# Optimization experiments

Hardware: AMD Instinct MI355X
Metric: run time of the kernel (lower is better)

Reference implementation:

```python
import jax, jax.numpy as jnp
import numpy as np

N = 2500   # total_neurons
K = 50     # connections_per_neuron
T = 60     # temporal_sequence
F = 5      # input_features
H = 128    # lstm hidden_size
B = 512    # batch
GROUPS = [800, 700, 600, 400]  # support_resistance, trend_detection, pattern_recognition, volume_analysis


def _lstm_layer(x, Wih, Whh, bih, bhh):
    # x: [B, T, D]; PyTorch gate order (i, f, g, o); eval mode (no dropout)
    bs = x.shape[0]
    h0 = jnp.zeros((bs, H), x.dtype)

    def step(carry, xt):
        h, c = carry
        g = xt @ Wih.T + h @ Whh.T + bih + bhh
        i, f, gg, o = jnp.split(g, 4, axis=-1)
        c = jax.nn.sigmoid(f) * c + jax.nn.sigmoid(i) * jnp.tanh(gg)
        h = jax.nn.sigmoid(o) * jnp.tanh(c)
        return (h, c), h

    (h, c), ys = jax.lax.scan(step, (h0, h0), jnp.swapaxes(x, 0, 1))
    return jnp.swapaxes(ys, 0, 1), h


def _forward(x, W_ih0, W_hh0, b_ih0, b_hh0, W_ih1, W_hh1, b_ih1, b_hh1,
             fp_w1, fp_b1, fp_w2, fp_b2, conn_w, sens, thr,
             int_w1, int_b1, int_w2, int_b2, int_w3, int_b3,
             tw, tb, pw, pb, kw, kb, vw, vb, cw, cb, conn_idx):
    y0, _ = _lstm_layer(x, W_ih0, W_hh0, b_ih0, b_hh0)
    _, hlast = _lstm_layer(y0, W_ih1, W_hh1, b_ih1, b_hh1)        # hidden[-1]: [B, H]
    base = jnp.tanh(jax.nn.relu(hlast @ fp_w1.T + fp_b1) @ fp_w2.T + fp_b2)  # [B, 32]
    # all_activations = base repeated over N neurons; each neuron reduces its
    # K gathered activations (weighted) and the identical 32 feature dims to a scalar.
    feat_sum = base.sum(-1)                                        # [B]
    acts = jnp.broadcast_to(feat_sum[:, None], (x.shape[0], N))    # [B, N]
    gathered = acts[:, conn_idx]                                   # [B, N, K] irregular gather
    wi = jnp.einsum('bnk,nk->bn', gathered, conn_w)                # [B, N]
    pre = wi * sens
    o0 = GROUPS[0]; o1 = o0 + GROUPS[1]; o2 = o1 + GROUPS[2]
    neuron_out = jnp.concatenate([
        jax.nn.sigmoid(pre[:, :o0] - thr[:o0]),                    # support_resistance
        jnp.tanh(pre[:, o0:o1]),                                   # trend_detection
        jax.nn.relu(pre[:, o1:o2] - thr[o1:o2]),                   # pattern_recognition
        jax.nn.sigmoid(pre[:, o2:]),                               # volume_analysis
    ], axis=1)                                                     # [B, N]
    h1 = jax.nn.relu(neuron_out @ int_w1.T + int_b1)
    h2 = jax.nn.relu(h1 @ int_w2.T + int_b2)
    integrated = jnp.tanh(h2 @ int_w3.T + int_b3)                  # [B, 32]
    trend = integrated @ tw.T + tb                                 # [B, 3]
    patt = integrated @ pw.T + pb                                  # [B, 6]
    keyl = integrated @ kw.T + kb                                  # [B, 4]
    vol = integrated @ vw.T + vb                                   # [B, 1]
    conf = integrated @ cw.T + cb                                  # [B, 1]
    means = jnp.stack([neuron_out[:, :o0].mean(1), neuron_out[:, o0:o1].mean(1),
                       neuron_out[:, o1:o2].mean(1), neuron_out[:, o2:].mean(1)], axis=-1)
    # heads(15) + raw confidence(1) + overall_confidence(1) + specialty means(4) -> [B, 21]? no: 3+6+4+1+1+1+4 = 20
    return jnp.concatenate([trend, patt, keyl, vol, conf, jax.nn.sigmoid(conf), means], axis=-1)


def setup_inputs() -> dict:
    key = jax.random.key(0)
    ks = jax.random.split(key, 40)
    rn = lambda k, s, sc=0.1: jax.random.normal(k, s, dtype=jnp.float32) * sc
    inp = {}
    inp['x'] = jax.random.normal(ks[0], (B, T, F), dtype=jnp.float32)
    inp['W_ih0'] = rn(ks[1], (4 * H, F)); inp['W_hh0'] = rn(ks[2], (4 * H, H))
    inp['b_ih0'] = rn(ks[3], (4 * H,));   inp['b_hh0'] = rn(ks[4], (4 * H,))
    inp['W_ih1'] = rn(ks[5], (4 * H, H)); inp['W_hh1'] = rn(ks[6], (4 * H, H))
    inp['b_ih1'] = rn(ks[7], (4 * H,));   inp['b_hh1'] = rn(ks[8], (4 * H,))
    inp['fp_w1'] = rn(ks[9], (64, H));    inp['fp_b1'] = rn(ks[10], (64,))
    inp['fp_w2'] = rn(ks[11], (32, 64));  inp['fp_b2'] = rn(ks[12], (32,))
    inp['conn_w'] = rn(ks[13], (N, K))
    inp['sens'] = 1.0 + rn(ks[14], (N,))
    inp['thr'] = 0.6 + rn(ks[15], (N,))
    inp['int_w1'] = rn(ks[16], (256, N), 0.02); inp['int_b1'] = rn(ks[17], (256,))
    inp['int_w2'] = rn(ks[18], (64, 256));      inp['int_b2'] = rn(ks[19], (64,))
    inp['int_w3'] = rn(ks[20], (32, 64));       inp['int_b3'] = rn(ks[21], (32,))
    inp['tw'] = rn(ks[22], (3, 32)); inp['tb'] = rn(ks[23], (3,))
    inp['pw'] = rn(ks[24], (6, 32)); inp['pb'] = rn(ks[25], (6,))
    inp['kw'] = rn(ks[26], (4, 32)); inp['kb'] = rn(ks[27], (4,))
    inp['vw'] = rn(ks[28], (1, 32)); inp['vb'] = rn(ks[29], (1,))
    inp['cw'] = rn(ks[30], (1, 32)); inp['cb'] = rn(ks[31], (1,))
    inp['conn_idx'] = jax.random.randint(ks[32], (N, K), 0, N)
    return inp


def reference(x, W_ih0, W_hh0, b_ih0, b_hh0, W_ih1, W_hh1, b_ih1, b_hh1,
              fp_w1, fp_b1, fp_w2, fp_b2, conn_w, sens, thr,
              int_w1, int_b1, int_w2, int_b2, int_w3, int_b3,
              tw, tb, pw, pb, kw, kb, vw, vb, cw, cb, conn_idx):
    return _forward(x, W_ih0, W_hh0, b_ih0, b_hh0, W_ih1, W_hh1, b_ih1, b_hh1,
                    fp_w1, fp_b1, fp_w2, fp_b2, conn_w, sens, thr,
                    int_w1, int_b1, int_w2, int_b2, int_w3, int_b3,
                    tw, tb, pw, pb, kw, kb, vw, vb, cw, cb, conn_idx)
```

## Files before the change

### kernel.cpp

```cpp
#include <hip/hip_runtime.h>
#include <math.h>

#define NB   512
#define TT   60
#define FF   5
#define HH   128
#define G4   512
#define NN   2500
#define KK   50

#define O0 800
#define O1 1500
#define O2 2100

#define OFF_B0F   0
#define OFF_B1F   40960
#define OFF_XA    106496
#define OFF_BIAS0 598016
#define OFF_BIAS1 598528
#define OFF_A     599040
#define OFF_FS    601540
#define OFF_MEANS 602052
#define OFF_H1    604100

#define PREP_T0 81920
#define PREP_T1 212992
#define PREP_T2 1196032
#define PREP_T3 1196544
#define PREP_T4 1197056
#define PREP_TOTAL 1199556

typedef _Float16 f16x8 __attribute__((ext_vector_type(8)));
typedef float f32x4 __attribute__((ext_vector_type(4)));

__device__ __forceinline__ float sigf(float x) {
    return 1.0f / (1.0f + __expf(-x));
}
__device__ __forceinline__ float tanh2(float x) {
    float e = __expf(-2.0f * x);
    return fmaf(2.0f, 1.0f / (1.0f + e), -1.0f);
}

__global__ __launch_bounds__(256) void prep_kernel(
    const float* __restrict__ x,
    const float* __restrict__ W_ih0, const float* __restrict__ W_hh0,
    const float* __restrict__ b_ih0, const float* __restrict__ b_hh0,
    const float* __restrict__ W_ih1, const float* __restrict__ W_hh1,
    const float* __restrict__ b_ih1, const float* __restrict__ b_hh1,
    const float* __restrict__ conn_w, const float* __restrict__ sens,
    float* __restrict__ ws)
{
    int i = blockIdx.x * 256 + threadIdx.x;
    if (i >= PREP_TOTAL) return;

    if (i < PREP_T0) {
        int j = i & 7, l = (i >> 3) & 63;
        int rest = i >> 9;
        int g = rest & 3;
        int kbw = rest >> 2;
        int kb = kbw % 5, w = kbw / 5;
        int k = kb * 32 + (l >> 4) * 8 + j;
        int n = g * 128 + w * 16 + (l & 15);
        float val = 0.f;
        if (k < 128)       val = W_hh0[n * HH + k];
        else if (k < 133)  val = W_ih0[n * FF + (k - 128)];
        ((_Float16*)(ws + OFF_B0F))[i] = (_Float16)val;
    } else if (i < PREP_T1) {
        int v = i - PREP_T0;
        int j = v & 7, l = (v >> 3) & 63;
        int rest = v >> 9;
        int g = rest & 3;
        int kb = (rest >> 2) & 7;
        int w = rest >> 5;
        int k = kb * 32 + (l >> 4) * 8 + j;
        int n = g * 128 + w * 16 + (l & 15);
        float val = (k < 128) ? W_ih1[n * HH + k] : W_hh1[n * HH + (k - 128)];
        ((_Float16*)(ws + OFF_B1F))[v] = (_Float16)val;
    } else if (i < PREP_T2) {
        int v = i - PREP_T1;
        int j = v & 7, l = (v >> 3) & 63;
        int rest = v >> 9;
        int t = rest % 60, bb = rest / 60;
        float val = 0.f;
        if (l < 16 && j < 5)
            val = x[(bb * 16 + (l & 15)) * (TT * FF) + t * FF + j];
        ((_Float16*)(ws + OFF_XA))[v] = (_Float16)val;
    } else if (i < PREP_T3) {
        int j = i - PREP_T2;
        ws[OFF_BIAS0 + j] = b_ih0[j] + b_hh0[j];
    } else if (i < PREP_T4) {
        int j = i - PREP_T3;
        ws[OFF_BIAS1 + j] = b_ih1[j] + b_hh1[j];
    } else {
        int n = i - PREP_T4;
        float s = 0.f;
        const float* cw = conn_w + n * KK;
        for (int k = 0; k < KK; ++k) s += cw[k];
        ws[OFF_A + n] = s * sens[n];
    }
}

__global__ __launch_bounds__(512) void lstm_mfma(
    const float* __restrict__ ws_ro,
    const float* __restrict__ fp_w1, const float* __restrict__ fp_b1,
    const float* __restrict__ fp_w2, const float* __restrict__ fp_b2,
    float* __restrict__ feat_sum)
{
    __shared__ __align__(16) _Float16 hcat[8 * 512];
    __shared__ float t1s[16][65];
    __shared__ float bss[16][33];

    const int tid = threadIdx.x;
    const int w = tid >> 6, l = tid & 63;
    const int u = w * 16 + (l & 15);
    const int row0 = (l >> 4) * 4;
    const int bb = blockIdx.x;

    ((uint4*)hcat)[tid] = make_uint4(0u, 0u, 0u, 0u);

    float bia0[4], bia1[4];
#pragma unroll
    for (int g = 0; g < 4; ++g) {
        bia0[g] = ws_ro[OFF_BIAS0 + g * 128 + u];
        bia1[g] = ws_ro[OFF_BIAS1 + g * 128 + u];
    }
    float c0[4] = {0.f, 0.f, 0.f, 0.f};
    float c1[4] = {0.f, 0.f, 0.f, 0.f};

    const f16x8* B0 = (const f16x8*)(ws_ro + OFF_B0F) + w * 20 * 64 + l;
    const f16x8* B1 = (const f16x8*)(ws_ro + OFF_B1F) + w * 32 * 64 + l;
    const f16x8* XA = (const f16x8*)(ws_ro + OFF_XA) + bb * 60 * 64 + l;
    const f16x8* HF = (const f16x8*)hcat;

    const int h0base = (u >> 5) * 512 + ((u >> 3) & 3) * 128 + (u & 7);
    const int h1base = h0base + 2048;

    __syncthreads();

    for (int t = 0; t < TT; ++t) {
        f32x4 a0 = {0.f,0.f,0.f,0.f}, a1 = {0.f,0.f,0.f,0.f};
        f32x4 a2 = {0.f,0.f,0.f,0.f}, a3 = {0.f,0.f,0.f,0.f};
        f16x8 xaf = XA[t * 64];
#pragma unroll
        for (int kb = 0; kb < 4; ++kb) {
            f16x8 af = HF[kb * 64 + l];
            a0 = __builtin_amdgcn_mfma_f32_16x16x32_f16(af, B0[(kb*4+0)*64], a0, 0,0,0);
            a1 = __builtin_amdgcn_mfma_f32_16x16x32_f16(af, B0[(kb*4+1)*64], a1, 0,0,0);
            a2 = __builtin_amdgcn_mfma_f32_16x16x32_f16(af, B0[(kb*4+2)*64], a2, 0,0,0);
            a3 = __builtin_amdgcn_mfma_f32_16x16x32_f16(af, B0[(kb*4+3)*64], a3, 0,0,0);
        }
        a0 = __builtin_amdgcn_mfma_f32_16x16x32_f16(xaf, B0[(16+0)*64], a0, 0,0,0);
        a1 = __builtin_amdgcn_mfma_f32_16x16x32_f16(xaf, B0[(16+1)*64], a1, 0,0,0);
        a2 = __builtin_amdgcn_mfma_f32_16x16x32_f16(xaf, B0[(16+2)*64], a2, 0,0,0);
        a3 = __builtin_amdgcn_mfma_f32_16x16x32_f16(xaf, B0[(16+3)*64], a3, 0,0,0);

        float h0v[4];
#pragma unroll
        for (int r = 0; r < 4; ++r) {
            float gi = sigf(a0[r] + bia0[0]);
            float gf = sigf(a1[r] + bia0[1]);
            float gg = tanh2(a2[r] + bia0[2]);
            float go = sigf(a3[r] + bia0[3]);
            c0[r] = gf * c0[r] + gi * gg;
            h0v[r] = go * tanh2(c0[r]);
        }
        __syncthreads();
#pragma unroll
        for (int r = 0; r < 4; ++r)
            hcat[h0base + (row0 + r) * 8] = (_Float16)h0v[r];
        __syncthreads();

        f32x4 b0a = {0.f,0.f,0.f,0.f}, b1a = {0.f,0.f,0.f,0.f};
        f32x4 b2a = {0.f,0.f,0.f,0.f}, b3a = {0.f,0.f,0.f,0.f};
#pragma unroll
        for (int kb = 0; kb < 8; ++kb) {
            f16x8 af = HF[kb * 64 + l];
            b0a = __builtin_amdgcn_mfma_f32_16x16x32_f16(af, B1[(kb*4+0)*64], b0a, 0,0,0);
            b1a = __builtin_amdgcn_mfma_f32_16x16x32_f16(af, B1[(kb*4+1)*64], b1a, 0,0,0);
            b2a = __builtin_amdgcn_mfma_f32_16x16x32_f16(af, B1[(kb*4+2)*64], b2a, 0,0,0);
            b3a = __builtin_amdgcn_mfma_f32_16x16x32_f16(af, B1[(kb*4+3)*64], b3a, 0,0,0);
        }
        float h1v[4];
#pragma unroll
        for (int r = 0; r < 4; ++r) {
            float gi = sigf(b0a[r] + bia1[0]);
            float gf = sigf(b1a[r] + bia1[1]);
            float gg = tanh2(b2a[r] + bia1[2]);
            float go = sigf(b3a[r] + bia1[3]);
            c1[r] = gf * c1[r] + gi * gg;
            h1v[r] = go * tanh2(c1[r]);
        }
        __syncthreads();
#pragma unroll
        for (int r = 0; r < 4; ++r)
            hcat[h1base + (row0 + r) * 8] = (_Float16)h1v[r];
        __syncthreads();
    }

    for (int idx = tid; idx < 16 * 64; idx += 512) {
        int r = idx >> 6, m = idx & 63;
        float acc = fp_b1[m];
        const float* wp = fp_w1 + m * HH;
        for (int k = 0; k < HH; ++k) {
            float hv = (float)hcat[(4 + (k >> 5)) * 512 +
                                   (r + ((k >> 3) & 3) * 16) * 8 + (k & 7)];
            acc = fmaf(wp[k], hv, acc);
        }
        t1s[r][m] = fmaxf(acc, 0.f);
    }
    __syncthreads();
    if (tid < 16 * 32) {
        int r = tid >> 5, q = tid & 31;
        float acc = fp_b2[q];
        const float* wp = fp_w2 + q * 64;
        for (int m = 0; m < 64; ++m) acc = fmaf(wp[m], t1s[r][m], acc);
        bss[r][q] = tanh2(acc);
    }
    __syncthreads();
    if (tid < 16) {
        float s = 0.f;
        for (int q = 0; q < 32; ++q) s += bss[tid][q];
        feat_sum[bb * 16 + tid] = s;
    }
}

__device__ __forceinline__ float actn(int n, float pre, float th) {
    if (n < O0)       return sigf(pre - th);
    else if (n < O1)  return tanh2(pre);
    else if (n < O2)  return fmaxf(pre - th, 0.f);
    else              return sigf(pre);
}

__global__ __launch_bounds__(256) void means_kernel(
    const float* __restrict__ feat_sum, const float* __restrict__ a,
    const float* __restrict__ thr, float* __restrict__ means)
{
    const int b = blockIdx.x;
    const float s = feat_sum[b];
    float g0 = 0.f, g1 = 0.f, g2 = 0.f, g3 = 0.f;
    for (int n = threadIdx.x; n < NN; n += 256) {
        float v = actn(n, s * a[n], thr[n]);
        if (n < O0) g0 += v; else if (n < O1) g1 += v;
        else if (n < O2) g2 += v; else g3 += v;
    }
    __shared__ float red[4][256];
    red[0][threadIdx.x] = g0; red[1][threadIdx.x] = g1;
    red[2][threadIdx.x] = g2; red[3][threadIdx.x] = g3;
    __syncthreads();
    if (threadIdx.x < 4) {
        float acc = 0.f;
        for (int i = 0; i < 256; ++i) acc += red[threadIdx.x][i];
        const float inv[4] = {1.f/800.f, 1.f/700.f, 1.f/600.f, 1.f/400.f};
        means[b * 4 + threadIdx.x] = acc * inv[threadIdx.x];
    }
}

__global__ __launch_bounds__(256) void gemm_h1(
    const float* __restrict__ feat_sum,
    const float* __restrict__ aw, const float* __restrict__ thr,
    const float* __restrict__ int_w1,
    const float* __restrict__ int_b1,
    float* __restrict__ h1)
{
    __shared__ float As[32][33];
    __shared__ float Bs[32][33];
    const int b0 = blockIdx.x * 32;
    const int m0 = blockIdx.y * 32;
    const int tid = threadIdx.x;
    const int ty = tid >> 4, tx = tid & 15;
    const int li = tid >> 3;
    const int lj = (tid & 7) * 4;

    const float s_li = feat_sum[b0 + li];

    float acc00 = 0.f, acc01 = 0.f, acc10 = 0.f, acc11 = 0.f;

    for (int k0 = 0; k0 < NN; k0 += 32) {
        float4 av = make_float4(0.f, 0.f, 0.f, 0.f);
        if (k0 + lj < NN) {
            float4 aa = *(const float4*)(aw + k0 + lj);
            float4 tt = *(const float4*)(thr + k0 + lj);
            int n = k0 + lj;
            av.x = actn(n + 0, s_li * aa.x, tt.x);
            av.y = actn(n + 1, s_li * aa.y, tt.y);
            av.z = actn(n + 2, s_li * aa.z, tt.z);
            av.w = actn(n + 3, s_li * aa.w, tt.w);
        }
        As[li][lj + 0] = av.x; As[li][lj + 1] = av.y;
        As[li][lj + 2] = av.z; As[li][lj + 3] = av.w;

        float4 wv = make_float4(0.f, 0.f, 0.f, 0.f);
        if (k0 + lj < NN)
            wv = *(const float4*)(int_w1 + (m0 + li) * NN + k0 + lj);
        Bs[lj + 0][li] = wv.x; Bs[lj + 1][li] = wv.y;
        Bs[lj + 2][li] = wv.z; Bs[lj + 3][li] = wv.w;
        __syncthreads();

#pragma unroll 8
        for (int kk = 0; kk < 32; ++kk) {
            float a0 = As[ty * 2][kk],  a1 = As[ty * 2 + 1][kk];
            float w0 = Bs[kk][tx * 2],  w1 = Bs[kk][tx * 2 + 1];
            acc00 += a0 * w0; acc01 += a0 * w1;
            acc10 += a1 * w0; acc11 += a1 * w1;
        }
        __syncthreads();
    }
    const int bi = b0 + ty * 2, mj = m0 + tx * 2;
    h1[bi * 256 + mj]           = fmaxf(acc00 + int_b1[mj], 0.f);
    h1[bi * 256 + mj + 1]       = fmaxf(acc01 + int_b1[mj + 1], 0.f);
    h1[(bi + 1) * 256 + mj]     = fmaxf(acc10 + int_b1[mj], 0.f);
    h1[(bi + 1) * 256 + mj + 1] = fmaxf(acc11 + int_b1[mj + 1], 0.f);
}

__global__ __launch_bounds__(64) void tail_kernel(
    const float* __restrict__ h1,
    const float* __restrict__ int_w2, const float* __restrict__ int_b2,
    const float* __restrict__ int_w3, const float* __restrict__ int_b3,
    const float* __restrict__ tw, const float* __restrict__ tb,
    const float* __restrict__ pw, const float* __restrict__ pb,
    const float* __restrict__ kw, const float* __restrict__ kb,
    const float* __restrict__ vw, const float* __restrict__ vb,
    const float* __restrict__ cw, const float* __restrict__ cb,
    const float* __restrict__ means,
    float* __restrict__ out)
{
    const int b = blockIdx.x;
    const int lane = threadIdx.x;
    __shared__ float h2s[64];
    __shared__ float ints[32];
    __shared__ float outs[16];

    {
        float acc = int_b2[lane];
        const float* hp = h1 + b * 256;
        const float* wp = int_w2 + lane * 256;
        for (int m = 0; m < 256; ++m) acc += wp[m] * hp[m];
        h2s[lane] = fmaxf(acc, 0.f);
    }
    __syncthreads();
    if (lane < 32) {
        float acc = int_b3[lane];
        const float* wp = int_w3 + lane * 64;
        for (int m = 0; m < 64; ++m) acc += wp[m] * h2s[m];
        ints[lane] = tanh2(acc);
    }
    __syncthreads();
    if (lane < 15) {
        const float* wsel; float bsel;
        if (lane < 3)       { wsel = tw + lane * 32;       bsel = tb[lane]; }
        else if (lane < 9)  { wsel = pw + (lane - 3) * 32; bsel = pb[lane - 3]; }
        else if (lane < 13) { wsel = kw + (lane - 9) * 32; bsel = kb[lane - 9]; }
        else if (lane == 13){ wsel = vw;                   bsel = vb[0]; }
        else                { wsel = cw;                   bsel = cb[0]; }
        float acc = bsel;
        for (int q = 0; q < 32; ++q) acc += wsel[q] * ints[q];
        outs[lane] = acc;
    }
    __syncthreads();
    if (lane < 20) {
        float v;
        if (lane < 15)       v = outs[lane];
        else if (lane == 15) v = sigf(outs[14]);
        else                 v = means[b * 4 + (lane - 16)];
        out[b * 20 + lane] = v;
    }
}

extern "C" void kernel_launch(void* const* d_in, const int* in_sizes, int n_in,
                              void* d_out, int out_size, void* d_ws, size_t ws_size,
                              hipStream_t stream)
{
    const float* x      = (const float*)d_in[0];
    const float* W_ih0  = (const float*)d_in[1];
    const float* W_hh0  = (const float*)d_in[2];
    const float* b_ih0  = (const float*)d_in[3];
    const float* b_hh0  = (const float*)d_in[4];
    const float* W_ih1  = (const float*)d_in[5];
    const float* W_hh1  = (const float*)d_in[6];
    const float* b_ih1  = (const float*)d_in[7];
    const float* b_hh1  = (const float*)d_in[8];
    const float* fp_w1  = (const float*)d_in[9];
    const float* fp_b1  = (const float*)d_in[10];
    const float* fp_w2  = (const float*)d_in[11];
    const float* fp_b2  = (const float*)d_in[12];
    const float* conn_w = (const float*)d_in[13];
    const float* sens   = (const float*)d_in[14];
    const float* thr    = (const float*)d_in[15];
    const float* int_w1 = (const float*)d_in[16];
    const float* int_b1 = (const float*)d_in[17];
    const float* int_w2 = (const float*)d_in[18];
    const float* int_b2 = (const float*)d_in[19];
    const float* int_w3 = (const float*)d_in[20];
    const float* int_b3 = (const float*)d_in[21];
    const float* tw     = (const float*)d_in[22];
    const float* tb     = (const float*)d_in[23];
    const float* pw     = (const float*)d_in[24];
    const float* pb     = (const float*)d_in[25];
    const float* kw     = (const float*)d_in[26];
    const float* kb     = (const float*)d_in[27];
    const float* vw     = (const float*)d_in[28];
    const float* vb     = (const float*)d_in[29];
    const float* cw     = (const float*)d_in[30];
    const float* cb     = (const float*)d_in[31];

    float* ws = (float*)d_ws;
    float* out = (float*)d_out;

    prep_kernel<<<(PREP_TOTAL + 255) / 256, 256, 0, stream>>>(
        x, W_ih0, W_hh0, b_ih0, b_hh0, W_ih1, W_hh1, b_ih1, b_hh1,
        conn_w, sens, ws);

    lstm_mfma<<<NB / 16, 512, 0, stream>>>(
        ws, fp_w1, fp_b1, fp_w2, fp_b2, ws + OFF_FS);

    means_kernel<<<NB, 256, 0, stream>>>(
        ws + OFF_FS, ws + OFF_A, thr, ws + OFF_MEANS);

    {
        dim3 grid(NB / 32, 256 / 32);
        gemm_h1<<<grid, 256, 0, stream>>>(
            ws + OFF_FS, ws + OFF_A, thr, int_w1, int_b1, ws + OFF_H1);
    }

    tail_kernel<<<NB, 64, 0, stream>>>(
        ws + OFF_H1, int_w2, int_b2, int_w3, int_b3,
        tw, tb, pw, pb, kw, kb, vw, vb, cw, cb,
        ws + OFF_MEANS, out);
}
```

Before: 392.4 us.

## Double-buffer LSTM hidden state, keep layer-0 weights in registers, fuse means into tail

The hidden-state LDS buffer is now double-buffered, so each LSTM timestep writes its h values directly after the gate math. That cuts the per-step barriers from four to two. Layer-0 weight fragments are kept in registers for the whole sequence, and layer-1 weight loads and the next input slice are prefetched one step ahead. The separate means kernel is removed and its reduction folded into the tail kernel, saving a launch. The risks are higher register pressure from the 20 cached fragments with the occupancy hint of two, and a smaller 64-thread block doing the 2500-neuron reduction.

```diff
diff --git a/kernel.cpp b/kernel.cpp
--- a/kernel.cpp
+++ b/kernel.cpp
@@ -20,8 +20,7 @@
 #define OFF_BIAS1 598528
 #define OFF_A     599040
 #define OFF_FS    601540
-#define OFF_MEANS 602052
-#define OFF_H1    604100
+#define OFF_H1    602052
 
 #define PREP_T0 81920
 #define PREP_T1 212992
@@ -100,13 +99,13 @@
     }
 }
 
-__global__ __launch_bounds__(512) void lstm_mfma(
+__global__ __launch_bounds__(512, 2) void lstm_mfma(
     const float* __restrict__ ws_ro,
     const float* __restrict__ fp_w1, const float* __restrict__ fp_b1,
     const float* __restrict__ fp_w2, const float* __restrict__ fp_b2,
     float* __restrict__ feat_sum)
 {
-    __shared__ __align__(16) _Float16 hcat[8 * 512];
+    __shared__ __align__(16) _Float16 hcat[2 * 4096];
     __shared__ float t1s[16][65];
     __shared__ float bss[16][33];
 
@@ -132,29 +131,41 @@
     const f16x8* XA = (const f16x8*)(ws_ro + OFF_XA) + bb * 60 * 64 + l;
     const f16x8* HF = (const f16x8*)hcat;
 
+    f16x8 wb0[20];
+#pragma unroll
+    for (int i = 0; i < 20; ++i) wb0[i] = B0[i * 64];
+
     const int h0base = (u >> 5) * 512 + ((u >> 3) & 3) * 128 + (u & 7);
     const int h1base = h0base + 2048;
 
-    __syncthreads();
-
-    for (int t = 0; t < TT; ++t) {
+    f16x8 xa = XA[0];
+
+    __syncthreads();
+
+    auto step = [&](int SRC, int DST, int t) {
+        const f16x8* hs = HF + SRC * 512;
+        const f16x8* hd = HF + DST * 512;
+        _Float16* hw = hcat + DST * 4096;
+
+        f16x8 xan = XA[(t + 1 < TT ? t + 1 : TT - 1) * 64];
+
         f32x4 a0 = {0.f,0.f,0.f,0.f}, a1 = {0.f,0.f,0.f,0.f};
         f32x4 a2 = {0.f,0.f,0.f,0.f}, a3 = {0.f,0.f,0.f,0.f};
-        f16x8 xaf = XA[t * 64];
 #pragma unroll
         for (int kb = 0; kb < 4; ++kb) {
-            f16x8 af = HF[kb * 64 + l];
-            a0 = __builtin_amdgcn_mfma_f32_16x16x32_f16(af, B0[(kb*4+0)*64], a0, 0,0,0);
-            a1 = __builtin_amdgcn_mfma_f32_16x16x32_f16(af, B0[(kb*4+1)*64], a1, 0,0,0);
-            a2 = __builtin_amdgcn_mfma_f32_16x16x32_f16(af, B0[(kb*4+2)*64], a2, 0,0,0);
-            a3 = __builtin_amdgcn_mfma_f32_16x16x32_f16(af, B0[(kb*4+3)*64], a3, 0,0,0);
-        }
-        a0 = __builtin_amdgcn_mfma_f32_16x16x32_f16(xaf, B0[(16+0)*64], a0, 0,0,0);
-        a1 = __builtin_amdgcn_mfma_f32_16x16x32_f16(xaf, B0[(16+1)*64], a1, 0,0,0);
-        a2 = __builtin_amdgcn_mfma_f32_16x16x32_f16(xaf, B0[(16+2)*64], a2, 0,0,0);
-        a3 = __builtin_amdgcn_mfma_f32_16x16x32_f16(xaf, B0[(16+3)*64], a3, 0,0,0);
-
-        float h0v[4];
+            f16x8 af = hs[kb * 64 + l];
+            a0 = __builtin_amdgcn_mfma_f32_16x16x32_f16(af, wb0[kb*4+0], a0, 0,0,0);
+            a1 = __builtin_amdgcn_mfma_f32_16x16x32_f16(af, wb0[kb*4+1], a1, 0,0,0);
+            a2 = __builtin_amdgcn_mfma_f32_16x16x32_f16(af, wb0[kb*4+2], a2, 0,0,0);
+            a3 = __builtin_amdgcn_mfma_f32_16x16x32_f16(af, wb0[kb*4+3], a3, 0,0,0);
+        }
+        a0 = __builtin_amdgcn_mfma_f32_16x16x32_f16(xa, wb0[16], a0, 0,0,0);
+        a1 = __builtin_amdgcn_mfma_f32_16x16x32_f16(xa, wb0[17], a1, 0,0,0);
+        a2 = __builtin_amdgcn_mfma_f32_16x16x32_f16(xa, wb0[18], a2, 0,0,0);
+        a3 = __builtin_amdgcn_mfma_f32_16x16x32_f16(xa, wb0[19], a3, 0,0,0);
+
+        f16x8 q0 = B1[0*64], q1 = B1[1*64], q2 = B1[2*64], q3 = B1[3*64];
+
 #pragma unroll
         for (int r = 0; r < 4; ++r) {
             float gi = sigf(a0[r] + bia0[0]);
@@ -162,39 +173,41 @@
             float gg = tanh2(a2[r] + bia0[2]);
             float go = sigf(a3[r] + bia0[3]);
             c0[r] = gf * c0[r] + gi * gg;
-            h0v[r] = go * tanh2(c0[r]);
+            hw[h0base + (row0 + r) * 8] = (_Float16)(go * tanh2(c0[r]));
         }
         __syncthreads();
-#pragma unroll
-        for (int r = 0; r < 4; ++r)
-            hcat[h0base + (row0 + r) * 8] = (_Float16)h0v[r];
+
+        f32x4 b0 = {0.f,0.f,0.f,0.f}, b1 = {0.f,0.f,0.f,0.f};
+        f32x4 b2 = {0.f,0.f,0.f,0.f}, b3 = {0.f,0.f,0.f,0.f};
+#pragma unroll
+        for (int kb = 0; kb < 8; ++kb) {
+            f16x8 af = (kb < 4) ? hd[kb * 64 + l] : hs[kb * 64 + l];
+            f16x8 p0 = q0, p1 = q1, p2 = q2, p3 = q3;
+            if (kb < 7) {
+                q0 = B1[((kb+1)*4+0)*64]; q1 = B1[((kb+1)*4+1)*64];
+                q2 = B1[((kb+1)*4+2)*64]; q3 = B1[((kb+1)*4+3)*64];
+            }
+            b0 = __builtin_amdgcn_mfma_f32_16x16x32_f16(af, p0, b0, 0,0,0);
+            b1 = __builtin_amdgcn_mfma_f32_16x16x32_f16(af, p1, b1, 0,0,0);
+            b2 = __builtin_amdgcn_mfma_f32_16x16x32_f16(af, p2, b2, 0,0,0);
+            b3 = __builtin_amdgcn_mfma_f32_16x16x32_f16(af, p3, b3, 0,0,0);
+        }
+#pragma unroll
+        for (int r = 0; r < 4; ++r) {
+            float gi = sigf(b0[r] + bia1[0]);
+            float gf = sigf(b1[r] + bia1[1]);
+            float gg = tanh2(b2[r] + bia1[2]);
+            float go = sigf(b3[r] + bia1[3]);
+            c1[r] = gf * c1[r] + gi * gg;
+            hw[h1base + (row0 + r) * 8] = (_Float16)(go * tanh2(c1[r]));
+        }
         __syncthreads();
-
-        f32x4 b0a = {0.f,0.f,0.f,0.f}, b1a = {0.f,0.f,0.f,0.f};
-        f32x4 b2a = {0.f,0.f,0.f,0.f}, b3a = {0.f,0.f,0.f,0.f};
-#pragma unroll
-        for (int kb = 0; kb < 8; ++kb) {
-            f16x8 af = HF[kb * 64 + l];
-            b0a = __builtin_amdgcn_mfma_f32_16x16x32_f16(af, B1[(kb*4+0)*64], b0a, 0,0,0);
-            b1a = __builtin_amdgcn_mfma_f32_16x16x32_f16(af, B1[(kb*4+1)*64], b1a, 0,0,0);
-            b2a = __builtin_amdgcn_mfma_f32_16x16x32_f16(af, B1[(kb*4+2)*64], b2a, 0,0,0);
-            b3a = __builtin_amdgcn_mfma_f32_16x16x32_f16(af, B1[(kb*4+3)*64], b3a, 0,0,0);
-        }
-        float h1v[4];
-#pragma unroll
-        for (int r = 0; r < 4; ++r) {
-            float gi = sigf(b0a[r] + bia1[0]);
-            float gf = sigf(b1a[r] + bia1[1]);
-            float gg = tanh2(b2a[r] + bia1[2]);
-            float go = sigf(b3a[r] + bia1[3]);
-            c1[r] = gf * c1[r] + gi * gg;
-            h1v[r] = go * tanh2(c1[r]);
-        }
-        __syncthreads();
-#pragma unroll
-        for (int r = 0; r < 4; ++r)
-            hcat[h1base + (row0 + r) * 8] = (_Float16)h1v[r];
-        __syncthreads();
+        xa = xan;
+    };
+
+    for (int t = 0; t < TT; t += 2) {
+        step(0, 1, t);
+        step(1, 0, t + 1);
     }
 
     for (int idx = tid; idx < 16 * 64; idx += 512) {
@@ -202,7 +215,7 @@
         float acc = fp_b1[m];
         const float* wp = fp_w1 + m * HH;
         for (int k = 0; k < HH; ++k) {
-            float hv = (float)hcat[(4 + (k >> 5)) * 512 +
+            float hv = (float)hcat[2048 + (k >> 5) * 512 +
                                    (r + ((k >> 3) & 3) * 16) * 8 + (k & 7)];
             acc = fmaf(wp[k], hv, acc);
         }
@@ -229,30 +242,6 @@
     else if (n < O1)  return tanh2(pre);
     else if (n < O2)  return fmaxf(pre - th, 0.f);
     else              return sigf(pre);
-}
-
-__global__ __launch_bounds__(256) void means_kernel(
-    const float* __restrict__ feat_sum, const float* __restrict__ a,
-    const float* __restrict__ thr, float* __restrict__ means)
-{
-    const int b = blockIdx.x;
-    const float s = feat_sum[b];
-    float g0 = 0.f, g1 = 0.f, g2 = 0.f, g3 = 0.f;
-    for (int n = threadIdx.x; n < NN; n += 256) {
-        float v = actn(n, s * a[n], thr[n]);
-        if (n < O0) g0 += v; else if (n < O1) g1 += v;
-        else if (n < O2) g2 += v; else g3 += v;
-    }
-    __shared__ float red[4][256];
-    red[0][threadIdx.x] = g0; red[1][threadIdx.x] = g1;
-    red[2][threadIdx.x] = g2; red[3][threadIdx.x] = g3;
-    __syncthreads();
-    if (threadIdx.x < 4) {
-        float acc = 0.f;
-        for (int i = 0; i < 256; ++i) acc += red[threadIdx.x][i];
-        const float inv[4] = {1.f/800.f, 1.f/700.f, 1.f/600.f, 1.f/400.f};
-        means[b * 4 + threadIdx.x] = acc * inv[threadIdx.x];
-    }
 }
 
 __global__ __launch_bounds__(256) void gemm_h1(
@@ -314,6 +303,8 @@
 
 __global__ __launch_bounds__(64) void tail_kernel(
     const float* __restrict__ h1,
+    const float* __restrict__ feat_sum,
+    const float* __restrict__ aw, const float* __restrict__ thr,
     const float* __restrict__ int_w2, const float* __restrict__ int_b2,
     const float* __restrict__ int_w3, const float* __restrict__ int_b3,
     const float* __restrict__ tw, const float* __restrict__ tb,
@@ -321,7 +312,6 @@
     const float* __restrict__ kw, const float* __restrict__ kb,
     const float* __restrict__ vw, const float* __restrict__ vb,
     const float* __restrict__ cw, const float* __restrict__ cb,
-    const float* __restrict__ means,
     float* __restrict__ out)
 {
     const int b = blockIdx.x;
@@ -329,6 +319,20 @@
     __shared__ float h2s[64];
     __shared__ float ints[32];
     __shared__ float outs[16];
+    __shared__ float red[4][64];
+    __shared__ float mred[4];
+
+    {
+        const float s = feat_sum[b];
+        float m0 = 0.f, m1 = 0.f, m2 = 0.f, m3 = 0.f;
+        for (int n = lane; n < NN; n += 64) {
+            float v = actn(n, s * aw[n], thr[n]);
+            if (n < O0) m0 += v; else if (n < O1) m1 += v;
+            else if (n < O2) m2 += v; else m3 += v;
+        }
+        red[0][lane] = m0; red[1][lane] = m1;
+        red[2][lane] = m2; red[3][lane] = m3;
+    }
 
     {
         float acc = int_b2[lane];
@@ -338,6 +342,12 @@
         h2s[lane] = fmaxf(acc, 0.f);
     }
     __syncthreads();
+    if (lane < 4) {
+        float acc = 0.f;
+        for (int i = 0; i < 64; ++i) acc += red[lane][i];
+        const float inv[4] = {1.f/800.f, 1.f/700.f, 1.f/600.f, 1.f/400.f};
+        mred[lane] = acc * inv[lane];
+    }
     if (lane < 32) {
         float acc = int_b3[lane];
         const float* wp = int_w3 + lane * 64;
@@ -361,7 +371,7 @@
         float v;
         if (lane < 15)       v = outs[lane];
         else if (lane == 15) v = sigf(outs[14]);
-        else                 v = means[b * 4 + (lane - 16)];
+        else                 v = mred[lane - 16];
         out[b * 20 + lane] = v;
     }
 }
@@ -413,9 +423,6 @@
     lstm_mfma<<<NB / 16, 512, 0, stream>>>(
         ws, fp_w1, fp_b1, fp_w2, fp_b2, ws + OFF_FS);
 
-    means_kernel<<<NB, 256, 0, stream>>>(
-        ws + OFF_FS, ws + OFF_A, thr, ws + OFF_MEANS);
-
     {
         dim3 grid(NB / 32, 256 / 32);
         gemm_h1<<<grid, 256, 0, stream>>>(
@@ -423,7 +430,8 @@
     }
 
     tail_kernel<<<NB, 64, 0, stream>>>(
-        ws + OFF_H1, int_w2, int_b2, int_w3, int_b3,
+        ws + OFF_H1, ws + OFF_FS, ws + OFF_A, thr,
+        int_w2, int_b2, int_w3, int_b3,
         tw, tb, pw, pb, kw, kb, vw, vb, cw, cb,
-        ws + OFF_MEANS, out);
-}
+        out);
+}
```

After: 428.4 us. +9.2%, slower.
